# Optimization experiments

Hardware: AMD Instinct MI355X
Metric: run time of the kernel (lower is better)

Reference implementation:

```python
import jax, jax.numpy as jnp
import numpy as np
from jax import lax

CAM_EDGE = 4096


def setup_inputs() -> dict:
    key = jax.random.key(0)
    x1 = jax.random.normal(key, (CAM_EDGE, CAM_EDGE), dtype=jnp.float32)
    return {"x1": x1}


def _label_components(mask):
    """4-connected component labeling via iterative min-label propagation.

    mask: [E, E] bool. Returns int32 [E, E] labels: each masked cell gets the
    minimum linear index of its connected component; unmasked cells get the
    sentinel N = E*E.
    """
    E = mask.shape[0]
    N = E * E
    sent = jnp.int32(N)
    init = jnp.where(mask, jnp.arange(N, dtype=jnp.int32).reshape(E, E), sent)
    sent_row = jnp.full((1, E), sent, dtype=jnp.int32)
    sent_col = jnp.full((E, 1), sent, dtype=jnp.int32)

    def propagate(lab):
        dn = jnp.concatenate([sent_row, lab[:-1]], axis=0)   # neighbor from above
        up = jnp.concatenate([lab[1:], sent_row], axis=0)    # neighbor from below
        lf = jnp.concatenate([sent_col, lab[:, :-1]], axis=1)
        rt = jnp.concatenate([lab[:, 1:], sent_col], axis=1)
        m = jnp.minimum(jnp.minimum(lab, up), jnp.minimum(dn, jnp.minimum(lf, rt)))
        return jnp.where(mask, m, sent)

    def cond(carry):
        _, changed = carry
        return changed

    def body(carry):
        lab, _ = carry
        new = propagate(lab)
        return new, jnp.any(new != lab)

    labels, _ = lax.while_loop(cond, body, (init, jnp.array(True)))
    return labels


def reference(x1):
    E = x1.shape[0]
    N = E * E
    v = jnp.tanh(x1)
    mask = v > 0
    labels = _label_components(mask)          # [E, E] int32, sentinel N for masked-out
    flat_lab = labels.reshape(-1)
    vflat = jnp.where(mask, v, 0.0).reshape(-1)
    ones = mask.reshape(-1).astype(v.dtype)
    # bucket N+1 collects the sentinel (non-positive cells); drop it
    sums = jax.ops.segment_sum(vflat, flat_lab, num_segments=N + 1)[:N]
    counts = jax.ops.segment_sum(ones, flat_lab, num_segments=N + 1)[:N]
    has = counts > 0                          # one True per connected component (its root index)
    per_comp = jnp.where(has, sums / (N + 1 - counts), 0.0)
    n_comp = jnp.sum(has.astype(v.dtype))
    total = jnp.sum(per_comp)
    return jnp.where(n_comp > 0, total / n_comp, 0.0)
```

## Files before the change

### kernel.cpp

```cpp
#include <hip/hip_runtime.h>

#define EDGE 4096
#define NPIX (EDGE * EDGE)
#define TILES_X 64
#define NTILES (TILES_X * TILES_X)
#define SLOTS 2048

typedef unsigned long long u64;

static __device__ __forceinline__ int g_load(int* L, int i) {
    return __hip_atomic_load(&L[i], __ATOMIC_RELAXED, __HIP_MEMORY_SCOPE_AGENT);
}
static __device__ __forceinline__ void g_store(int* L, int i, int v) {
    __hip_atomic_store(&L[i], v, __ATOMIC_RELAXED, __HIP_MEMORY_SCOPE_AGENT);
}
static __device__ int g_find(int* L, int i) {
    while (true) {
        const int p = g_load(L, i);
        if (p == i) return i;
        const int gp = g_load(L, p);
        if (gp == p) return p;
        g_store(L, i, gp);
        i = gp;
    }
}
static __device__ int g_unite(int* L, int a, int b) {
    while (true) {
        a = g_find(L, a); b = g_find(L, b);
        if (a == b) return 0;
        const int lo = a < b ? a : b;
        const int hi = a ^ b ^ lo;
        const int old = atomicMin(&L[hi], lo);
        if (old == hi) return 1;
        a = lo; b = old;
    }
}

static __device__ __forceinline__ int l_load(int* L, int i) {
    return __hip_atomic_load(&L[i], __ATOMIC_RELAXED, __HIP_MEMORY_SCOPE_WORKGROUP);
}
static __device__ __forceinline__ void l_store(int* L, int i, int v) {
    __hip_atomic_store(&L[i], v, __ATOMIC_RELAXED, __HIP_MEMORY_SCOPE_WORKGROUP);
}
static __device__ int l_find(int* L, int i) {
    while (true) {
        const int p = l_load(L, i);
        if (p == i) return i;
        const int gp = l_load(L, p);
        if (gp == p) return p;
        l_store(L, i, gp);
        i = gp;
    }
}
static __device__ void l_unite(int* L, int a, int b) {
    while (true) {
        a = l_find(L, a); b = l_find(L, b);
        if (a == b) return;
        const int lo = a < b ? a : b;
        const int hi = a ^ b ^ lo;
        const int old = atomicMin(&L[hi], lo);
        if (old == hi) return;
        a = lo; b = old;
    }
}

__global__ __launch_bounds__(256) void k_tile(const float* __restrict__ x,
                                              int* __restrict__ G,
                                              int* __restrict__ topM, int* __restrict__ botM,
                                              int* __restrict__ leftM, int* __restrict__ rightM,
                                              int* __restrict__ rootsArr,
                                              double* __restrict__ partials) {
    __shared__ u64 mrow[64];
    __shared__ u64 rstart[64];
    __shared__ unsigned int mpart[64][4];
    __shared__ int rowbase[64];
    __shared__ int P[SLOTS];
    __shared__ int wtot[4];
    __shared__ double wsum[4];
    __shared__ int Rtot;
    const int t = threadIdx.x;
    const int tile = blockIdx.x;
    const int tr = tile >> 6, tc = tile & 63;

    const int r = t >> 2, qd = t & 3;
    const float4* xp = reinterpret_cast<const float4*>(
        x + ((size_t)((tr << 6) | r) << 12) + (tc << 6) + (qd << 4));
    unsigned int m16 = 0;
    float sf = 0.0f;
    #pragma unroll
    for (int k = 0; k < 4; ++k) {
        const float4 a = xp[k];
        const float vv[4] = {a.x, a.y, a.z, a.w};
        #pragma unroll
        for (int j = 0; j < 4; ++j) {
            const float v = vv[j];
            if (v > 0.0f) {
                m16 |= 1u << (k * 4 + j);
                const float e = __expf(2.0f * v);
                sf += 1.0f - 2.0f / (e + 1.0f);
            }
        }
    }
    mpart[r][qd] = m16;
    double s = (double)sf;
    for (int off = 32; off > 0; off >>= 1) s += __shfl_down(s, off, 64);
    if ((t & 63) == 0) wsum[t >> 6] = s;
    __syncthreads();

    if (t < 64) {
        const u64 m = (u64)mpart[t][0] | ((u64)mpart[t][1] << 16)
                    | ((u64)mpart[t][2] << 32) | ((u64)mpart[t][3] << 48);
        mrow[t] = m;
        const u64 rs = m & ~(m << 1);
        rstart[t] = rs;
        int inc = __popcll(rs);
        const int nr = inc;
        #pragma unroll
        for (int off = 1; off < 64; off <<= 1) {
            const int v = __shfl_up(inc, off, 64);
            if (t >= off) inc += v;
        }
        rowbase[t] = inc - nr;
        if (t == 63) Rtot = inc;
    }
    __syncthreads();

    const int R = Rtot;
    const int tileBase = tile * SLOTS;
    {
        int rr, j;
        if (t < 64)       { rr = 0;       j = t; }
        else if (t < 128) { rr = 63;      j = t - 64; }
        else if (t < 192) { rr = t - 128; j = 0; }
        else              { rr = t - 192; j = 63; }
        int node = -1;
        if ((mrow[rr] >> j) & 1ull) {
            const int idx = __popcll(rstart[rr] & (~0ull >> (63 - j))) - 1;
            node = tileBase + rowbase[rr] + idx;
        }
        const int bi = (tile << 6) | (t & 63);
        if (t < 64)       topM[bi]   = node;
        else if (t < 128) botM[bi]   = node;
        else if (t < 192) leftM[bi]  = node;
        else              rightM[bi] = node;
    }
    for (int i = t; i < R; i += 256) P[i] = i;
    if (t == 0) partials[tile] = wsum[0] + wsum[1] + wsum[2] + wsum[3];
    __syncthreads();

    {
        const int rr = t >> 2;
        if (rr >= 1) {
            const u64 vm = mrow[rr] & mrow[rr - 1];
            u64 st = vm & ~(vm << 1);
            const int cb = (t & 3) * 16;
            st = (st >> cb) & 0xFFFFull;
            if (st) {
                const u64 rs  = rstart[rr];
                const u64 rsu = rstart[rr - 1];
                const int rb  = rowbase[rr];
                const int rbu = rowbase[rr - 1];
                do {
                    const int j = __builtin_ctzll(st) + cb;
                    const u64 thru = ~0ull >> (63 - j);
                    l_unite(P, rb  + __popcll(rs  & thru) - 1,
                               rbu + __popcll(rsu & thru) - 1);
                    st &= st - 1;
                } while (st);
            }
        }
    }
    __syncthreads();

    int c = 0;
    for (int i = t; i < R; i += 256) {
        const int pi = P[i];
        c += (pi == i);
        G[tileBase + i] = tileBase + pi;
    }
    for (int off = 32; off > 0; off >>= 1) c += __shfl_down(c, off, 64);
    if ((t & 63) == 0) wtot[t >> 6] = c;
    __syncthreads();
    if (t == 0) rootsArr[tile] = wtot[0] + wtot[1] + wtot[2] + wtot[3];
}

__global__ __launch_bounds__(128) void k_xmerge(const int* __restrict__ topM,
                                                const int* __restrict__ botM,
                                                const int* __restrict__ leftM,
                                                const int* __restrict__ rightM,
                                                int* G, int* __restrict__ linksArr) {
    __shared__ int lsum[2];
    const int t = threadIdx.x, tile = blockIdx.x;
    const int tr = tile >> 6, tc = tile & 63;
    int links = 0;
    if (t < 64) {
        if (tr > 0) {
            const int a = topM[(tile << 6) | t];
            const int b = botM[((tile - 64) << 6) | t];
            const int ap = __shfl_up(a, 1, 64);
            const int bp = __shfl_up(b, 1, 64);
            if ((a | b) >= 0) {
                const bool redund = (t > 0) && ((ap | bp) >= 0);
                if (!redund) links = g_unite(G, a, b);
            }
        }
    } else {
        const int rr = t - 64;
        if (tc > 0) {
            const int a = leftM[(tile << 6) | rr];
            const int b = rightM[((tile - 1) << 6) | rr];
            const int ap = __shfl_up(a, 1, 64);
            const int bp = __shfl_up(b, 1, 64);
            if ((a | b) >= 0) {
                const bool redund = (rr > 0) && ((ap | bp) >= 0);
                if (!redund) links = g_unite(G, a, b);
            }
        }
    }
    for (int off = 32; off > 0; off >>= 1) links += __shfl_down(links, off, 64);
    if ((t & 63) == 0) lsum[t >> 6] = links;
    __syncthreads();
    if (t == 0) linksArr[tile] = lsum[0] + lsum[1];
}

__global__ __launch_bounds__(256) void k_final(const double* __restrict__ partials,
                                               const int* __restrict__ rootsArr,
                                               const int* __restrict__ linksArr,
                                               float* __restrict__ out) {
    __shared__ double sd[256];
    __shared__ int si[256];
    const int t = threadIdx.x;
    double s = 0.0; int n = 0;
    for (int i = t; i < NTILES; i += 256) {
        s += partials[i];
        n += rootsArr[i] - linksArr[i];
    }
    sd[t] = s; si[t] = n; __syncthreads();
    for (int off = 128; off > 0; off >>= 1) {
        if (t < off) { sd[t] += sd[t + off]; si[t] += si[t + off]; }
        __syncthreads();
    }
    if (t == 0) {
        const int nn = si[0];
        out[0] = (nn > 0) ? (float)(sd[0] / (double)(NPIX + 1) / (double)nn) : 0.0f;
    }
}

extern "C" void kernel_launch(void* const* d_in, const int* in_sizes, int n_in,
                              void* d_out, int out_size, void* d_ws, size_t ws_size,
                              hipStream_t stream) {
    const float* x = (const float*)d_in[0];
    float* out = (float*)d_out;

    char* ws = (char*)d_ws;
    int* G = (int*)ws;
    int* topM   = (int*)(ws + (32u << 20));
    int* botM   = topM  + NTILES * 64;
    int* leftM  = botM  + NTILES * 64;
    int* rightM = leftM + NTILES * 64;
    double* partials = (double*)(ws + (36u << 20));
    int* rootsArr = (int*)(ws + (36u << 20) + (64u << 10));
    int* linksArr = (int*)(ws + (36u << 20) + (80u << 10));

    k_tile  <<<NTILES, 256, 0, stream>>>(x, G, topM, botM, leftM, rightM,
                                         rootsArr, partials);
    k_xmerge<<<NTILES, 128, 0, stream>>>(topM, botM, leftM, rightM, G, linksArr);
    k_final <<<1, 256, 0, stream>>>(partials, rootsArr, linksArr, out);
}
```

Before: 62.36 us.

## Compact per-tile roots and export border labels as compacted root ids

The local tile pass now relabels union-find roots into a compact range and writes global parent entries only for those roots, not for every run. Border node ids are resolved to their local root before being exported, which removes one barrier and shrinks later global find work. The union step first tries an atomicMin on the lower node before falling back to a full unite. P initialisation now fills all slots, and the tanh division uses a hardware reciprocal, which trades a little accuracy for speed.

Result: faster. 56.08 us (-10.1%).

```diff
diff --git a/kernel.cpp b/kernel.cpp
--- a/kernel.cpp
+++ b/kernel.cpp
@@ -97,7 +97,7 @@
             if (v > 0.0f) {
                 m16 |= 1u << (k * 4 + j);
                 const float e = __expf(2.0f * v);
-                sf += 1.0f - 2.0f / (e + 1.0f);
+                sf += 1.0f - 2.0f * __builtin_amdgcn_rcpf(e + 1.0f);
             }
         }
     }
@@ -123,28 +123,8 @@
         rowbase[t] = inc - nr;
         if (t == 63) Rtot = inc;
     }
-    __syncthreads();
-
-    const int R = Rtot;
-    const int tileBase = tile * SLOTS;
-    {
-        int rr, j;
-        if (t < 64)       { rr = 0;       j = t; }
-        else if (t < 128) { rr = 63;      j = t - 64; }
-        else if (t < 192) { rr = t - 128; j = 0; }
-        else              { rr = t - 192; j = 63; }
-        int node = -1;
-        if ((mrow[rr] >> j) & 1ull) {
-            const int idx = __popcll(rstart[rr] & (~0ull >> (63 - j))) - 1;
-            node = tileBase + rowbase[rr] + idx;
-        }
-        const int bi = (tile << 6) | (t & 63);
-        if (t < 64)       topM[bi]   = node;
-        else if (t < 128) botM[bi]   = node;
-        else if (t < 192) leftM[bi]  = node;
-        else              rightM[bi] = node;
-    }
-    for (int i = t; i < R; i += 256) P[i] = i;
+    #pragma unroll
+    for (int i = t; i < SLOTS; i += 256) P[i] = i;
     if (t == 0) partials[tile] = wsum[0] + wsum[1] + wsum[2] + wsum[3];
     __syncthreads();
 
@@ -163,8 +143,10 @@
                 do {
                     const int j = __builtin_ctzll(st) + cb;
                     const u64 thru = ~0ull >> (63 - j);
-                    l_unite(P, rb  + __popcll(rs  & thru) - 1,
-                               rbu + __popcll(rsu & thru) - 1);
+                    const int na = rb  + __popcll(rs  & thru) - 1;
+                    const int nb = rbu + __popcll(rsu & thru) - 1;
+                    const int old = atomicMin(&P[na], nb);
+                    if (old != na && old != nb) l_unite(P, nb, old);
                     st &= st - 1;
                 } while (st);
             }
@@ -172,16 +154,54 @@
     }
     __syncthreads();
 
+    const int R = Rtot;
+    int broot = -1;
+    {
+        int rr, j;
+        if (t < 64)       { rr = 0;       j = t; }
+        else if (t < 128) { rr = 63;      j = t - 64; }
+        else if (t < 192) { rr = t - 128; j = 0; }
+        else              { rr = t - 192; j = 63; }
+        if ((mrow[rr] >> j) & 1ull) {
+            const int idx = __popcll(rstart[rr] & (~0ull >> (63 - j))) - 1;
+            broot = l_find(P, rowbase[rr] + idx);
+        }
+    }
     int c = 0;
-    for (int i = t; i < R; i += 256) {
-        const int pi = P[i];
-        c += (pi == i);
-        G[tileBase + i] = tileBase + pi;
-    }
-    for (int off = 32; off > 0; off >>= 1) c += __shfl_down(c, off, 64);
-    if ((t & 63) == 0) wtot[t >> 6] = c;
-    __syncthreads();
-    if (t == 0) rootsArr[tile] = wtot[0] + wtot[1] + wtot[2] + wtot[3];
+    for (int i = t; i < R; i += 256) c += (P[i] == i);
+    int inc2 = c;
+    #pragma unroll
+    for (int off = 1; off < 64; off <<= 1) {
+        const int v = __shfl_up(inc2, off, 64);
+        if ((t & 63) >= off) inc2 += v;
+    }
+    if ((t & 63) == 63) wtot[t >> 6] = inc2;
+    __syncthreads();
+
+    const int w = t >> 6;
+    int wbase = 0;
+    if (w > 0) wbase += wtot[0];
+    if (w > 1) wbase += wtot[1];
+    if (w > 2) wbase += wtot[2];
+    const int my_base = wbase + inc2 - c;
+    const int nroots = wtot[0] + wtot[1] + wtot[2] + wtot[3];
+    const int tileBase = tile * SLOTS;
+    {
+        int k = my_base;
+        for (int i = t; i < R; i += 256) if (P[i] == i) P[i] = k++;
+    }
+    for (int i = t; i < nroots; i += 256) G[tileBase + i] = tileBase + i;
+    __syncthreads();
+
+    {
+        const int node = (broot >= 0) ? (tileBase + P[broot]) : -1;
+        const int bi = (tile << 6) | (t & 63);
+        if (t < 64)       topM[bi]   = node;
+        else if (t < 128) botM[bi]   = node;
+        else if (t < 192) leftM[bi]  = node;
+        else              rightM[bi] = node;
+    }
+    if (t == 0) rootsArr[tile] = nroots;
 }
 
 __global__ __launch_bounds__(128) void k_xmerge(const int* __restrict__ topM,
```
